# Performance work log

Hardware: AMD Instinct MI355X
Metric: run time of the kernel (lower is better)

Reference implementation:

```python
import jax, jax.numpy as jnp
import numpy as np

EMBED_DIM = 512
NUM_HEADS = 8
HEAD_DIM = EMBED_DIM // NUM_HEADS
SEQ = 1024
BSZ = 8
T1 = 0.6
T2 = 0.4
MAX_NEG = -jnp.finfo(jnp.float32).max


def setup_inputs() -> dict:
    key = jax.random.key(0)
    ks = jax.random.split(key, 10)
    shp = (SEQ, BSZ, EMBED_DIM)
    inv = 1.0 / np.sqrt(EMBED_DIM)
    return {
        "query": jax.random.normal(ks[0], shp, jnp.float32),
        "key": jax.random.normal(ks[1], shp, jnp.float32),
        "value": jax.random.normal(ks[2], shp, jnp.float32),
        "query_sem": jax.random.normal(ks[3], shp, jnp.float32),
        "key_sem": jax.random.normal(ks[4], shp, jnp.float32),
        "sem_map": jax.random.uniform(ks[5], (SEQ, SEQ), jnp.float32),
        "in_proj_weight": jax.random.normal(ks[6], (3 * EMBED_DIM, EMBED_DIM), jnp.float32) * inv,
        "in_proj_bias": jnp.zeros((3 * EMBED_DIM,), jnp.float32),
        "out_proj_weight": jax.random.normal(ks[7], (EMBED_DIM, EMBED_DIM), jnp.float32) * inv,
        "out_proj_bias": jnp.zeros((EMBED_DIM,), jnp.float32),
    }


def _heads(x):
    # [T, B, E] -> [B*H, T, head_dim]
    T, B, E = x.shape
    return jnp.transpose(x.reshape(T, B * NUM_HEADS, HEAD_DIM), (1, 0, 2))


def _attn_path(qx, kx, vx, sem_map, Wi, bi, Wo, bo, ssa):
    # packed in-projection (generic path: q, k, v are distinct tensors)
    Wq, Wk, Wv = jnp.split(Wi, 3, axis=0)
    bq, bk, bv = jnp.split(bi, 3)
    q = _heads(qx @ Wq.T + bq)
    k = _heads(kx @ Wk.T + bk)
    v = _heads(vx @ Wv.T + bv)
    scale = 1.0 / np.sqrt(HEAD_DIM)
    scores = jnp.einsum("bte,bse->bts", q * scale, k)  # [B*H, T, S]
    scores = jnp.where(sem_map[None, :, :] < 0.5, MAX_NEG, scores)
    if ssa:
        # keep only the argmax entry per row, others set to max_neg
        idx = jnp.argmax(scores, axis=-1)  # [B*H, T]
        keep = jnp.arange(scores.shape[-1])[None, None, :] == idx[..., None]
        scores = jnp.where(keep, scores, MAX_NEG)
    w = jax.nn.softmax(scores, axis=-1)
    o = jnp.einsum("bts,bse->bte", w, v)  # [B*H, T, head_dim]
    o = jnp.transpose(o, (1, 0, 2)).reshape(SEQ, BSZ, EMBED_DIM)
    return o @ Wo.T + bo


def reference(query, key, value, query_sem, key_sem, sem_map, in_proj_weight, in_proj_bias, out_proj_weight, out_proj_bias):
    # SCA: semantic q/k attend, style value
    x_sca = _attn_path(query_sem, key_sem, value, sem_map, in_proj_weight, in_proj_bias, out_proj_weight, out_proj_bias, ssa=False)
    # SSA: content/style q/k, hard-argmax sparsified attention
    x_ssa = _attn_path(query, key, value, sem_map, in_proj_weight, in_proj_bias, out_proj_weight, out_proj_bias, ssa=True)
    return T1 * x_sca + T2 * x_ssa
```

## Files before the change

kernel.cpp:

```cpp
#include <hip/hip_runtime.h>
#include <float.h>


namespace {
constexpr int kSeq = 1024;
constexpr int kBsz = 8;
constexpr int kEmb = 512;
constexpr int kHD  = 64;
constexpr float kT1 = 0.6f;
constexpr float kT2 = 0.4f;
constexpr float kScale = 0.125f;
constexpr float kMargin = 0.125f;
constexpr int kCap = 256;
}

typedef short bf16x8 __attribute__((ext_vector_type(8)));
typedef float f32x4  __attribute__((ext_vector_type(4)));

union FragU { uint4 u4; bf16x8 f; uint u[4]; };

__device__ __forceinline__ ushort f2bf(float f) {
  uint u = __float_as_uint(f);
  u += 0x7fff + ((u >> 16) & 1);
  return (ushort)(u >> 16);
}
__device__ __forceinline__ uint pack2(float lo, float hi) {
  return (uint)f2bf(lo) | ((uint)f2bf(hi) << 16);
}
__device__ __forceinline__ float bf2f(uint h) {
  return __uint_as_float(h << 16);
}
__device__ __forceinline__ uint monokey(float v) {
  uint u = __float_as_uint(v);
  return (u & 0x80000000u) ? ~u : (u | 0x80000000u);
}

__global__ void smask_prep(const float* __restrict__ SEM,
                           unsigned long long* __restrict__ SMASK) {
  const int t = blockIdx.x;
  const int w4 = threadIdx.x >> 6;
  const int lane = threadIdx.x & 63;
#pragma unroll
  for (int i = 0; i < 4; ++i) {
    const int word = (w4 << 2) + i;
    const float v = SEM[t * kSeq + (word << 6) + lane];
    unsigned long long m = __ballot(v >= 0.5f);
    if (lane == 0) SMASK[t * 16 + word] = m;
  }
}

__global__ __launch_bounds__(256, 4) void proj_v2(
    const float* __restrict__ X, const float* __restrict__ W,
    const float* __restrict__ bias, float* __restrict__ Out,
    int woff, ushort* __restrict__ shadow, float sscale)
{
  __shared__ float As[32 * 132];
  __shared__ float Bs[32 * 68];

  const int mBase = blockIdx.x << 7;
  const int nBase = blockIdx.y << 6;
  const int tid = threadIdx.x;
  const int tx = tid & 15;
  const int my = tid >> 4;
  const int ar = tid >> 1, ah = (tid & 1) << 4;
  const int br = tid >> 2, bk = (tid & 3) << 3;

  float acc[8][4];
#pragma unroll
  for (int i = 0; i < 8; ++i)
#pragma unroll
    for (int j = 0; j < 4; ++j) acc[i][j] = 0.f;

  const float* xp = X + (size_t)(mBase + ar) * kEmb + ah;
  const float* wp = W + (size_t)(woff + nBase + br) * kEmb + bk;

  for (int k0 = 0; k0 < kEmb; k0 += 32) {
    float4 a0 = ((const float4*)(xp + k0))[0];
    float4 a1 = ((const float4*)(xp + k0))[1];
    float4 a2 = ((const float4*)(xp + k0))[2];
    float4 a3 = ((const float4*)(xp + k0))[3];
    float4 b0 = ((const float4*)(wp + k0))[0];
    float4 b1 = ((const float4*)(wp + k0))[1];
    __syncthreads();
    {
      float av[16] = {a0.x, a0.y, a0.z, a0.w, a1.x, a1.y, a1.z, a1.w,
                      a2.x, a2.y, a2.z, a2.w, a3.x, a3.y, a3.z, a3.w};
#pragma unroll
      for (int i = 0; i < 16; ++i) As[(ah + i) * 132 + ar] = av[i];
      float bv[8] = {b0.x, b0.y, b0.z, b0.w, b1.x, b1.y, b1.z, b1.w};
#pragma unroll
      for (int i = 0; i < 8; ++i) Bs[(bk + i) * 68 + br] = bv[i];
    }
    __syncthreads();

#pragma unroll 8
    for (int k = 0; k < 32; ++k) {
      float4 A0 = *(const float4*)&As[k * 132 + (my << 3)];
      float4 A1 = *(const float4*)&As[k * 132 + (my << 3) + 4];
      float4 Bv = *(const float4*)&Bs[k * 68 + (tx << 2)];
      float aa[8] = {A0.x, A0.y, A0.z, A0.w, A1.x, A1.y, A1.z, A1.w};
      float bb[4] = {Bv.x, Bv.y, Bv.z, Bv.w};
#pragma unroll
      for (int i = 0; i < 8; ++i)
#pragma unroll
        for (int j = 0; j < 4; ++j)
          acc[i][j] = fmaf(aa[i], bb[j], acc[i][j]);
    }
  }

#pragma unroll
  for (int i = 0; i < 8; ++i) {
    const int m = mBase + (my << 3) + i;
#pragma unroll
    for (int j = 0; j < 4; ++j) {
      const int n = nBase + (tx << 2) + j;
      const float v = acc[i][j] + bias[woff + n];
      const int oi = (((m & 7) << 3) + (n >> 6)) * (kSeq * kHD) +
                     ((m >> 3) << 6) + (n & 63);
      Out[oi] = v;
      shadow[oi] = f2bf(v * sscale);
    }
  }
}

__global__ __launch_bounds__(256, 2) void gemm_bf16(
    const float* __restrict__ X, const ushort* __restrict__ X16,
    const float* __restrict__ W, const float* __restrict__ bias,
    float* __restrict__ OutF, ushort* __restrict__ Out16,
    int woff, int aMode, int outMode, float scale)
{
  __shared__ uint As[128 * 20];
  __shared__ uint Bs[64 * 20];

  const int mBase = blockIdx.x << 7;
  const int nBase = blockIdx.y << 6;
  const int tid = threadIdx.x;
  const int w = tid >> 6;
  const int l = tid & 63;
  const int l15 = l & 15;
  const int quad = l >> 4;
  const int wm = w & 1, wn = w >> 1;

  const int srow = tid >> 1;
  const int shalf = tid & 1;

  f32x4 acc[4][2];
#pragma unroll
  for (int mi = 0; mi < 4; ++mi)
#pragma unroll
    for (int ni = 0; ni < 2; ++ni) acc[mi][ni] = (f32x4){0.f, 0.f, 0.f, 0.f};

  for (int k0 = 0; k0 < kEmb; k0 += 32) {
    uint4 ah0, ah1;
    if (aMode == 2) {
      const uint* src = (const uint*)X16 + (size_t)(mBase + srow) * 256 +
                        (k0 >> 1) + (shalf << 3);
      ah0 = ((const uint4*)src)[0];
      ah1 = ((const uint4*)src)[1];
    } else {
      const float* xp = X + (size_t)(mBase + srow) * kEmb + k0 + (shalf << 4);
      float4 f0 = ((const float4*)xp)[0];
      float4 f1 = ((const float4*)xp)[1];
      float4 f2 = ((const float4*)xp)[2];
      float4 f3 = ((const float4*)xp)[3];
      ah0 = make_uint4(pack2(f0.x, f0.y), pack2(f0.z, f0.w),
                       pack2(f1.x, f1.y), pack2(f1.z, f1.w));
      ah1 = make_uint4(pack2(f2.x, f2.y), pack2(f2.z, f2.w),
                       pack2(f3.x, f3.y), pack2(f3.z, f3.w));
    }
    uint4 bw0, bw1;
    if (tid < 128) {
      const float* wp = W + (size_t)(woff + nBase + srow) * kEmb + k0 + (shalf << 4);
      float4 f0 = ((const float4*)wp)[0];
      float4 f1 = ((const float4*)wp)[1];
      float4 f2 = ((const float4*)wp)[2];
      float4 f3 = ((const float4*)wp)[3];
      bw0 = make_uint4(pack2(f0.x, f0.y), pack2(f0.z, f0.w),
                       pack2(f1.x, f1.y), pack2(f1.z, f1.w));
      bw1 = make_uint4(pack2(f2.x, f2.y), pack2(f2.z, f2.w),
                       pack2(f3.x, f3.y), pack2(f3.z, f3.w));
    }
    __syncthreads();
    {
      uint* dst = As + srow * 20 + (shalf << 3);
      ((uint4*)dst)[0] = ah0;
      ((uint4*)dst)[1] = ah1;
      if (tid < 128) {
        uint* db = Bs + srow * 20 + (shalf << 3);
        ((uint4*)db)[0] = bw0;
        ((uint4*)db)[1] = bw1;
      }
    }
    __syncthreads();

    FragU aF[4], bF[2];
#pragma unroll
    for (int ni = 0; ni < 2; ++ni)
      bF[ni].u4 = *(const uint4*)(Bs + ((wn << 5) + (ni << 4) + l15) * 20 + (quad << 2));
#pragma unroll
    for (int mi = 0; mi < 4; ++mi)
      aF[mi].u4 = *(const uint4*)(As + ((wm << 6) + (mi << 4) + l15) * 20 + (quad << 2));
#pragma unroll
    for (int mi = 0; mi < 4; ++mi)
#pragma unroll
      for (int ni = 0; ni < 2; ++ni)
        acc[mi][ni] = __builtin_amdgcn_mfma_f32_16x16x32_bf16(
            aF[mi].f, bF[ni].f, acc[mi][ni], 0, 0, 0);
  }

#pragma unroll
  for (int ni = 0; ni < 2; ++ni) {
    const int n = nBase + (wn << 5) + (ni << 4) + l15;
    const float bv = bias[woff + n];
#pragma unroll
    for (int mi = 0; mi < 4; ++mi) {
#pragma unroll
      for (int r = 0; r < 4; ++r) {
        const int m = mBase + (wm << 6) + (mi << 4) + (quad << 2) + r;
        const float v = acc[mi][ni][r] + bv;
        if (outMode == 0) {
          OutF[(size_t)m * kEmb + n] = v;
        } else {
          const int oi = (((m & 7) << 3) + (n >> 6)) * (kSeq * kHD) +
                         ((m >> 3) << 6) + (n & 63);
          Out16[oi] = f2bf(v * scale);
        }
      }
    }
  }
}

__global__ __launch_bounds__(256, 4) void sca_mfma2(
    const ushort* __restrict__ Q16, const ushort* __restrict__ K16,
    const ushort* __restrict__ V16,
    const unsigned long long* __restrict__ SMASK,
    ushort* __restrict__ MIX16)
{
  __shared__ uint ks[64 * 36];
  __shared__ uint vt[64 * 36];
  __shared__ uint ps[4][16 * 36];

  const int t0  = blockIdx.x << 6;
  const int bh  = blockIdx.y;
  const int tid = threadIdx.x;
  const int w    = tid >> 6;
  const int l    = tid & 63;
  const int l15  = l & 15;
  const int quad = l >> 4;

  const uint* Qu = (const uint*)Q16 + (size_t)bh * (kSeq * 32);
  const uint* Ku = (const uint*)K16 + (size_t)bh * (kSeq * 32);
  const uint* Vu = (const uint*)V16 + (size_t)bh * (kSeq * 32);

  FragU qf0, qf1;
  {
    const uint* qrow = Qu + (size_t)(t0 + (w << 4) + l15) * 32;
    qf0.u4 = *(const uint4*)(qrow + (quad << 2));
    qf1.u4 = *(const uint4*)(qrow + 16 + (quad << 2));
  }

  f32x4 oacc[4];
#pragma unroll
  for (int nt = 0; nt < 4; ++nt) oacc[nt] = (f32x4){0.f, 0.f, 0.f, 0.f};
  float den[4] = {0.f, 0.f, 0.f, 0.f};

  uint* psw = ps[w];

  for (int s0 = 0, tile = 0; s0 < kSeq; s0 += 64, ++tile) {
    __syncthreads();
    {
      const int sl = tid >> 2, c = tid & 3;
      const uint* kp = Ku + (size_t)(s0 + sl) * 32 + (c << 3);
      uint4 a = ((const uint4*)kp)[0];
      uint4 b = ((const uint4*)kp)[1];
      uint* dst = ks + sl * 36 + (c << 3);
      ((uint4*)dst)[0] = a;
      ((uint4*)dst)[1] = b;
    }
    {
      const int p = tid >> 3, c7 = tid & 7;
      const uint* va = Vu + (size_t)(s0 + (p << 1)) * 32 + (c7 << 2);
      FragU A, B;
      A.u4 = *(const uint4*)va;
      B.u4 = *(const uint4*)(va + 32);
      const int Wp = (p + ((c7 & 3) << 2)) & 31;
#pragma unroll
      for (int i = 0; i < 8; ++i) {
        uint ai = (A.u[i >> 1] >> ((i & 1) << 4)) & 0xFFFF;
        uint bi = (B.u[i >> 1] >> ((i & 1) << 4)) & 0xFFFF;
        vt[((c7 << 3) + i) * 36 + Wp] = ai | (bi << 16);
      }
    }
    __syncthreads();

    unsigned long long wv[4];
#pragma unroll
    for (int r = 0; r < 4; ++r)
      wv[r] = SMASK[(size_t)(t0 + (w << 4) + (quad << 2) + r) * 16 + tile];

#pragma unroll
    for (int st = 0; st < 4; ++st) {
      f32x4 sacc = (f32x4){0.f, 0.f, 0.f, 0.f};
      const int srow = (st << 4) + l15;
      FragU kf0, kf1;
      kf0.u4 = *(const uint4*)(ks + srow * 36 + (quad << 2));
      kf1.u4 = *(const uint4*)(ks + srow * 36 + 16 + (quad << 2));
      sacc = __builtin_amdgcn_mfma_f32_16x16x32_bf16(qf0.f, kf0.f, sacc, 0, 0, 0);
      sacc = __builtin_amdgcn_mfma_f32_16x16x32_bf16(qf1.f, kf1.f, sacc, 0, 0, 0);

#pragma unroll
      for (int r = 0; r < 4; ++r) {
        const int trow = (quad << 2) + r;
        const uint bit = (uint)(wv[r] >> ((st << 4) + l15)) & 1u;
        const float val = bit ? __expf(sacc[r]) : 0.f;
        den[r] += val;
        const int W  = (st << 3) + (l15 >> 1);
        const int Wp = (W + (((trow >> 3) & 1) << 3)) & 31;
        ushort* p16 = (ushort*)(psw + trow * 36 + Wp);
        p16[l15 & 1] = f2bf(val);
      }
    }
#pragma unroll
    for (int ch = 0; ch < 2; ++ch) {
      FragU pf;
      const int pw = ((ch << 4) + (quad << 2) + (((l15 >> 3) & 1) << 3)) & 31;
      pf.u4 = *(const uint4*)(psw + l15 * 36 + pw);
#pragma unroll
      for (int nt = 0; nt < 4; ++nt) {
        const int d = (nt << 4) + l15;
        const int vw = ((ch << 4) + (quad << 2) + (((d >> 3) & 3) << 2)) & 31;
        FragU vf;
        vf.u4 = *(const uint4*)(vt + d * 36 + vw);
        oacc[nt] = __builtin_amdgcn_mfma_f32_16x16x32_bf16(pf.f, vf.f, oacc[nt], 0, 0, 0);
      }
    }
  }

#pragma unroll
  for (int r = 0; r < 4; ++r) {
    float d = den[r];
    d += __shfl_xor(d, 1);
    d += __shfl_xor(d, 2);
    d += __shfl_xor(d, 4);
    d += __shfl_xor(d, 8);
    den[r] = kT1 / d;
  }
  const int b = bh >> 3, h = bh & 7;
#pragma unroll
  for (int nt = 0; nt < 4; ++nt) {
#pragma unroll
    for (int r = 0; r < 4; ++r) {
      const int t = t0 + (w << 4) + (quad << 2) + r;
      const int d = (nt << 4) + l15;
      MIX16[(size_t)(t * kBsz + b) * kEmb + (h << 6) + d] =
          f2bf(oacc[nt][r] * den[r]);
    }
  }
}

__global__ __launch_bounds__(512, 2) void ssa_v3(
    const ushort* __restrict__ Q16, const ushort* __restrict__ K16,
    const float* __restrict__ Qf, const float* __restrict__ Kf,
    const ushort* __restrict__ V16,
    const unsigned long long* __restrict__ SMASK,
    ushort* __restrict__ MIX16)
{
  __shared__ uint ks[64 * 36];
  __shared__ uint2 list[8][kCap];
  __shared__ float thrL[8][16];
  __shared__ unsigned long long key64L[8][16];
  __shared__ uint cnt[8];

  const int t0  = blockIdx.x << 7;
  const int bh  = blockIdx.y;
  const int tid = threadIdx.x;
  const int w    = tid >> 6;
  const int l    = tid & 63;
  const int l15  = l & 15;
  const int quad = l >> 4;

  if (tid < 8) cnt[tid] = 0;
  if (tid < 128) ((unsigned long long*)key64L)[tid] = 0ull;

  const uint* Qu = (const uint*)Q16 + (size_t)bh * (kSeq * 32);
  const uint* Ku = (const uint*)K16 + (size_t)bh * (kSeq * 32);

  FragU qf0, qf1;
  {
    const uint* qrow = Qu + (size_t)(t0 + (w << 4) + l15) * 32;
    qf0.u4 = *(const uint4*)(qrow + (quad << 2));
    qf1.u4 = *(const uint4*)(qrow + 16 + (quad << 2));
  }

  float m4[4] = {-FLT_MAX, -FLT_MAX, -FLT_MAX, -FLT_MAX};

  for (int s0 = 0, tile = 0; s0 < kSeq; s0 += 64, ++tile) {
    __syncthreads();
    {
      const int row = tid >> 3, c = tid & 7;
      uint4 a = *(const uint4*)(Ku + (size_t)(s0 + row) * 32 + (c << 2));
      *(uint4*)(ks + row * 36 + (c << 2)) = a;
    }
    __syncthreads();

    unsigned long long wv[4];
#pragma unroll
    for (int r = 0; r < 4; ++r)
      wv[r] = SMASK[(size_t)(t0 + (w << 4) + (quad << 2) + r) * 16 + tile];

    f32x4 sv[4];
#pragma unroll
    for (int st = 0; st < 4; ++st) {
      f32x4 sacc = (f32x4){0.f, 0.f, 0.f, 0.f};
      const int srow = (st << 4) + l15;
      FragU kf0, kf1;
      kf0.u4 = *(const uint4*)(ks + srow * 36 + (quad << 2));
      kf1.u4 = *(const uint4*)(ks + srow * 36 + 16 + (quad << 2));
      sacc = __builtin_amdgcn_mfma_f32_16x16x32_bf16(qf0.f, kf0.f, sacc, 0, 0, 0);
      sacc = __builtin_amdgcn_mfma_f32_16x16x32_bf16(qf1.f, kf1.f, sacc, 0, 0, 0);
      sv[st] = sacc;
#pragma unroll
      for (int r = 0; r < 4; ++r) {
        const uint bit = (uint)(wv[r] >> ((st << 4) + l15)) & 1u;
        if (bit) m4[r] = fmaxf(m4[r], sacc[r]);
      }
    }
#pragma unroll
    for (int r = 0; r < 4; ++r) {
      float m = m4[r];
      m = fmaxf(m, __shfl_xor(m, 1));
      m = fmaxf(m, __shfl_xor(m, 2));
      m = fmaxf(m, __shfl_xor(m, 4));
      m = fmaxf(m, __shfl_xor(m, 8));
      m4[r] = m;
    }
#pragma unroll
    for (int st = 0; st < 4; ++st) {
#pragma unroll
      for (int r = 0; r < 4; ++r) {
        const uint bit = (uint)(wv[r] >> ((st << 4) + l15)) & 1u;
        const float x = sv[st][r];
        if (bit && x >= m4[r] - kMargin) {
          uint idx = atomicAdd(&cnt[w], 1u);
          if (idx < (uint)kCap) {
            const int rowid = (quad << 2) + r;
            const int s = s0 + (st << 4) + l15;
            list[w][idx] = make_uint2(__float_as_uint(x),
                                      ((uint)rowid << 10) | (uint)s);
          }
        }
      }
    }
  }

  if (l15 == 0) {
#pragma unroll
    for (int r = 0; r < 4; ++r) thrL[w][(quad << 2) + r] = m4[r] - kMargin;
  }
  __syncthreads();

  const uint n = min(cnt[w], (uint)kCap);
  const float* Qbf = Qf + (size_t)bh * (kSeq * kHD);
  const float* Kbf = Kf + (size_t)bh * (kSeq * kHD);
  for (uint base = 0; base < n; base += 64) {
    const uint e = base + (uint)l;
    if (e < n) {
      const uint2 ent = list[w][e];
      const uint rowid = ent.y >> 10;
      const uint s = ent.y & 1023u;
      const float xv = __uint_as_float(ent.x);
      if (xv >= thrL[w][rowid]) {
        const int t = t0 + (w << 4) + (int)rowid;
        const float* qe = Qbf + (size_t)t * kHD;
        const float* ke = Kbf + (size_t)s * kHD;
        float p0 = 0.f, p1 = 0.f, p2 = 0.f, p3 = 0.f;
#pragma unroll
        for (int i = 0; i < 16; ++i) {
          float4 qq = *(const float4*)(qe + (i << 2));
          float4 kk = *(const float4*)(ke + (i << 2));
          p0 = fmaf(qq.x, kk.x, p0);
          p1 = fmaf(qq.y, kk.y, p1);
          p2 = fmaf(qq.z, kk.z, p2);
          p3 = fmaf(qq.w, kk.w, p3);
        }
        const float acc = ((p0 + p1) + (p2 + p3)) * kScale;
        const unsigned long long key =
            ((unsigned long long)monokey(acc) << 16) |
            (unsigned long long)(1023u - s);
        atomicMax(&key64L[w][rowid], key);
      }
    }
  }
  __syncthreads();

  const int b = bh >> 3, h = bh & 7;
  const uint* Vu = (const uint*)V16 + (size_t)bh * (kSeq * 32);
#pragma unroll
  for (int r = 0; r < 4; ++r) {
    const int rowid = (quad << 2) + r;
    const unsigned long long key = key64L[w][rowid];
    const uint s = 1023u - (uint)(key & 0xFFFFull);
    const uint2 vv = *(const uint2*)(Vu + (size_t)s * 32 + (l15 << 1));
    const int t = t0 + (w << 4) + rowid;
    uint* op = (uint*)MIX16 + ((size_t)(t * kBsz + b) * kEmb + (h << 6)) / 2 + (l15 << 1);
    uint2 o = *(uint2*)op;
    float o0 = bf2f(o.x & 0xFFFF) + kT2 * bf2f(vv.x & 0xFFFF);
    float o1 = bf2f(o.x >> 16)    + kT2 * bf2f(vv.x >> 16);
    float o2 = bf2f(o.y & 0xFFFF) + kT2 * bf2f(vv.y & 0xFFFF);
    float o3 = bf2f(o.y >> 16)    + kT2 * bf2f(vv.y >> 16);
    *(uint2*)op = make_uint2(pack2(o0, o1), pack2(o2, o3));
  }
}

extern "C" void kernel_launch(void* const* d_in, const int* in_sizes, int n_in,
                              void* d_out, int out_size, void* d_ws, size_t ws_size,
                              hipStream_t stream) {
  const float* query  = (const float*)d_in[0];
  const float* key    = (const float*)d_in[1];
  const float* value  = (const float*)d_in[2];
  const float* qsem   = (const float*)d_in[3];
  const float* ksem   = (const float*)d_in[4];
  const float* semmap = (const float*)d_in[5];
  const float* Wi     = (const float*)d_in[6];
  const float* bi     = (const float*)d_in[7];
  const float* Wo     = (const float*)d_in[8];
  const float* bo     = (const float*)d_in[9];
  float* out = (float*)d_out;

  char* ws = (char*)d_ws;
  unsigned long long* SMASK = (unsigned long long*)ws;          ws += 1024 * 16 * 8;
  ushort* Q16  = (ushort*)ws;  ws += (size_t)64 * kSeq * kHD * 2;
  ushort* K16  = (ushort*)ws;  ws += (size_t)64 * kSeq * kHD * 2;
  ushort* V16  = (ushort*)ws;  ws += (size_t)64 * kSeq * kHD * 2;
  ushort* MIX16 = (ushort*)ws; ws += (size_t)kSeq * kBsz * kEmb * 2;
  float* P1 = (float*)ws;      ws += (size_t)64 * kSeq * kHD * 4;
  float* P0 = out;

  const dim3 gp(64, 8);
  const dim3 gb(64, 8);
  const dim3 gs(16, 64);
  const dim3 gv(8, 64);

  smask_prep<<<1024, 256, 0, stream>>>(semmap, SMASK);
  gemm_bf16<<<gb, 256, 0, stream>>>(qsem, nullptr, Wi, bi, nullptr, Q16,
                                    0, 0, 1, kScale);
  gemm_bf16<<<gb, 256, 0, stream>>>(ksem, nullptr, Wi, bi, nullptr, K16,
                                    512, 0, 1, 1.0f);
  gemm_bf16<<<gb, 256, 0, stream>>>(value, nullptr, Wi, bi, nullptr, V16,
                                    1024, 0, 1, 1.0f);
  sca_mfma2<<<gs, 256, 0, stream>>>(Q16, K16, V16, SMASK, MIX16);
  proj_v2<<<gp, 256, 0, stream>>>(query, Wi, bi, P0, 0,   Q16, kScale);
  proj_v2<<<gp, 256, 0, stream>>>(key,   Wi, bi, P1, 512, K16, 1.0f);
  ssa_v3<<<gv, 512, 0, stream>>>(Q16, K16, P0, P1, V16, SMASK, MIX16);
  gemm_bf16<<<gb, 256, 0, stream>>>(nullptr, MIX16, Wo, bo, out, nullptr,
                                    0, 2, 0, 1.0f);
}
```

Measured before the change: 449.3 us.

## Batch projection launches via grid z and load fp32 A tile directly to registers

Merges the three semantic/value bf16 projection GEMMs into one launch over blockIdx.z, and the two fp32 content projections into one proj_v3 launch. proj_v3 also drops the shared-memory A tile: each thread streams its eight rows straight from global memory into registers, double-buffered, while the B tile is prefetched one step ahead. This aims to cut launch overhead and the tail effect of small grids, and to remove LDS transposes and one barrier per k-step. The trade-off is uncoalesced strided global loads for A, more register pressure, and reliance on cache hits for the reused A rows.

```diff
diff --git a/kernel.cpp b/kernel.cpp
--- a/kernel.cpp
+++ b/kernel.cpp
@@ -49,20 +49,26 @@
   }
 }
 
-__global__ __launch_bounds__(256, 4) void proj_v2(
-    const float* __restrict__ X, const float* __restrict__ W,
-    const float* __restrict__ bias, float* __restrict__ Out,
-    int woff, ushort* __restrict__ shadow, float sscale)
+__global__ __launch_bounds__(256, 4) void proj_v3(
+    const float* __restrict__ Xq, const float* __restrict__ Xk,
+    const float* __restrict__ W, const float* __restrict__ bias,
+    float* __restrict__ OutQ, float* __restrict__ OutK,
+    ushort* __restrict__ ShQ, ushort* __restrict__ ShK)
 {
-  __shared__ float As[32 * 132];
   __shared__ float Bs[32 * 68];
+
+  const int z = blockIdx.z;
+  const float* X = z ? Xk : Xq;
+  float* Out = z ? OutK : OutQ;
+  ushort* shadow = z ? ShK : ShQ;
+  const int woff = z << 9;
+  const float sscale = z ? 1.0f : kScale;
 
   const int mBase = blockIdx.x << 7;
   const int nBase = blockIdx.y << 6;
   const int tid = threadIdx.x;
   const int tx = tid & 15;
   const int my = tid >> 4;
-  const int ar = tid >> 1, ah = (tid & 1) << 4;
   const int br = tid >> 2, bk = (tid & 3) << 3;
 
   float acc[8][4];
@@ -71,42 +77,64 @@
 #pragma unroll
     for (int j = 0; j < 4; ++j) acc[i][j] = 0.f;
 
-  const float* xp = X + (size_t)(mBase + ar) * kEmb + ah;
+  const float* xrow = X + (size_t)(mBase + (my << 3)) * kEmb;
   const float* wp = W + (size_t)(woff + nBase + br) * kEmb + bk;
 
+  float4 Acur[8], Anxt[8];
+
+#define LOADQ(dst, kk) do {                                              \
+    const int kc_ = ((kk) < kEmb) ? (kk) : 0;                            \
+    _Pragma("unroll")                                                    \
+    for (int i_ = 0; i_ < 8; ++i_)                                       \
+      dst[i_] = *(const float4*)(xrow + (size_t)i_ * kEmb + kc_);        \
+  } while (0)
+
+#define FMAQ(src, qq) do {                                               \
+    _Pragma("unroll")                                                    \
+    for (int kk_ = 0; kk_ < 4; ++kk_) {                                  \
+      const float4 Bv_ =                                                 \
+          *(const float4*)&Bs[(((qq) << 2) + kk_) * 68 + (tx << 2)];     \
+      _Pragma("unroll")                                                  \
+      for (int i_ = 0; i_ < 8; ++i_) {                                   \
+        const float a_ = (kk_ == 0) ? src[i_].x : (kk_ == 1) ? src[i_].y \
+                       : (kk_ == 2) ? src[i_].z : src[i_].w;             \
+        acc[i_][0] = fmaf(a_, Bv_.x, acc[i_][0]);                        \
+        acc[i_][1] = fmaf(a_, Bv_.y, acc[i_][1]);                        \
+        acc[i_][2] = fmaf(a_, Bv_.z, acc[i_][2]);                        \
+        acc[i_][3] = fmaf(a_, Bv_.w, acc[i_][3]);                        \
+      }                                                                  \
+    }                                                                    \
+  } while (0)
+
+  LOADQ(Acur, 0);
+  float4 b0 = ((const float4*)wp)[0];
+  float4 b1 = ((const float4*)wp)[1];
+
   for (int k0 = 0; k0 < kEmb; k0 += 32) {
-    float4 a0 = ((const float4*)(xp + k0))[0];
-    float4 a1 = ((const float4*)(xp + k0))[1];
-    float4 a2 = ((const float4*)(xp + k0))[2];
-    float4 a3 = ((const float4*)(xp + k0))[3];
-    float4 b0 = ((const float4*)(wp + k0))[0];
-    float4 b1 = ((const float4*)(wp + k0))[1];
     __syncthreads();
     {
-      float av[16] = {a0.x, a0.y, a0.z, a0.w, a1.x, a1.y, a1.z, a1.w,
-                      a2.x, a2.y, a2.z, a2.w, a3.x, a3.y, a3.z, a3.w};
-#pragma unroll
-      for (int i = 0; i < 16; ++i) As[(ah + i) * 132 + ar] = av[i];
       float bv[8] = {b0.x, b0.y, b0.z, b0.w, b1.x, b1.y, b1.z, b1.w};
 #pragma unroll
       for (int i = 0; i < 8; ++i) Bs[(bk + i) * 68 + br] = bv[i];
     }
-    __syncthreads();
-
-#pragma unroll 8
-    for (int k = 0; k < 32; ++k) {
-      float4 A0 = *(const float4*)&As[k * 132 + (my << 3)];
-      float4 A1 = *(const float4*)&As[k * 132 + (my << 3) + 4];
-      float4 Bv = *(const float4*)&Bs[k * 68 + (tx << 2)];
-      float aa[8] = {A0.x, A0.y, A0.z, A0.w, A1.x, A1.y, A1.z, A1.w};
-      float bb[4] = {Bv.x, Bv.y, Bv.z, Bv.w};
-#pragma unroll
-      for (int i = 0; i < 8; ++i)
-#pragma unroll
-        for (int j = 0; j < 4; ++j)
-          acc[i][j] = fmaf(aa[i], bb[j], acc[i][j]);
-    }
-  }
+    {
+      const int kn = (k0 + 32 < kEmb) ? k0 + 32 : 0;
+      b0 = ((const float4*)(wp + kn))[0];
+      b1 = ((const float4*)(wp + kn))[1];
+    }
+    __syncthreads();
+
+#pragma unroll
+    for (int qp = 0; qp < 4; ++qp) {
+      const int q0 = qp << 1;
+      LOADQ(Anxt, k0 + ((q0 + 1) << 2));
+      FMAQ(Acur, q0);
+      LOADQ(Acur, k0 + ((q0 + 2) << 2));
+      FMAQ(Anxt, q0 + 1);
+    }
+  }
+#undef LOADQ
+#undef FMAQ
 
 #pragma unroll
   for (int i = 0; i < 8; ++i) {
@@ -124,13 +152,20 @@
 }
 
 __global__ __launch_bounds__(256, 2) void gemm_bf16(
-    const float* __restrict__ X, const ushort* __restrict__ X16,
+    const float* __restrict__ X0, const float* __restrict__ X1,
+    const float* __restrict__ X2, const ushort* __restrict__ X16,
     const float* __restrict__ W, const float* __restrict__ bias,
     float* __restrict__ OutF, ushort* __restrict__ Out16,
-    int woff, int aMode, int outMode, float scale)
+    int woffBase, int aMode, int outMode, float scale0)
 {
   __shared__ uint As[128 * 20];
   __shared__ uint Bs[64 * 20];
+
+  const int z = blockIdx.z;
+  const float* X = (z == 0) ? X0 : (z == 1) ? X1 : X2;
+  const int woff = woffBase + (z << 9);
+  const float scale = (z == 0) ? scale0 : 1.0f;
+  const size_t zoff = (size_t)z * ((size_t)kSeq * kBsz * kEmb);
 
   const int mBase = blockIdx.x << 7;
   const int nBase = blockIdx.y << 6;
@@ -223,7 +258,7 @@
         } else {
           const int oi = (((m & 7) << 3) + (n >> 6)) * (kSeq * kHD) +
                          ((m >> 3) << 6) + (n & 63);
-          Out16[oi] = f2bf(v * scale);
+          Out16[zoff + oi] = f2bf(v * scale);
         }
       }
     }
@@ -536,22 +571,18 @@
   float* P1 = (float*)ws;      ws += (size_t)64 * kSeq * kHD * 4;
   float* P0 = out;
 
-  const dim3 gp(64, 8);
+  const dim3 gp(64, 8, 2);
+  const dim3 g3(64, 8, 3);
   const dim3 gb(64, 8);
   const dim3 gs(16, 64);
   const dim3 gv(8, 64);
 
   smask_prep<<<1024, 256, 0, stream>>>(semmap, SMASK);
-  gemm_bf16<<<gb, 256, 0, stream>>>(qsem, nullptr, Wi, bi, nullptr, Q16,
-                                    0, 0, 1, kScale);
-  gemm_bf16<<<gb, 256, 0, stream>>>(ksem, nullptr, Wi, bi, nullptr, K16,
-                                    512, 0, 1, 1.0f);
-  gemm_bf16<<<gb, 256, 0, stream>>>(value, nullptr, Wi, bi, nullptr, V16,
-                                    1024, 0, 1, 1.0f);
+  gemm_bf16<<<g3, 256, 0, stream>>>(qsem, ksem, value, nullptr, Wi, bi,
+                                    nullptr, Q16, 0, 0, 1, kScale);
   sca_mfma2<<<gs, 256, 0, stream>>>(Q16, K16, V16, SMASK, MIX16);
-  proj_v2<<<gp, 256, 0, stream>>>(query, Wi, bi, P0, 0,   Q16, kScale);
-  proj_v2<<<gp, 256, 0, stream>>>(key,   Wi, bi, P1, 512, K16, 1.0f);
+  proj_v3<<<gp, 256, 0, stream>>>(query, key, Wi, bi, P0, P1, Q16, K16);
   ssa_v3<<<gv, 512, 0, stream>>>(Q16, K16, P0, P1, V16, SMASK, MIX16);
-  gemm_bf16<<<gb, 256, 0, stream>>>(nullptr, MIX16, Wo, bo, out, nullptr,
-                                    0, 2, 0, 1.0f);
-}
+  gemm_bf16<<<gb, 256, 0, stream>>>(nullptr, nullptr, nullptr, MIX16, Wo, bo,
+                                    out, nullptr, 0, 2, 0, 1.0f);
+}
```

New measurement: 470.5 us. 1.05x slower.
